# Kernel tuning notes

Hardware: AMD Instinct MI355X
Metric: run time of the kernel (lower is better)

## Reference

```python
import jax, jax.numpy as jnp
import numpy as np

N = 50000      # nodes
E = 800000     # edges
D = 128        # in_dim == out_dim
H = 8          # heads
DH = D // H    # head dim = 16
BN_EPS = 1e-5


def batch_norm(x, gamma, beta):
    # BatchNorm1d in training mode: biased variance over the node/batch axis.
    mu = jnp.mean(x, axis=0)
    var = jnp.mean((x - mu) ** 2, axis=0)
    return (x - mu) * jax.lax.rsqrt(var + BN_EPS) * gamma + beta


def setup_inputs() -> dict:
    key = jax.random.key(0)
    ks = jax.random.split(key, 16)
    inp = {
        'src': jax.random.randint(ks[0], (E,), 0, N),
        'dst': jax.random.randint(ks[1], (E,), 0, N),
        'h': jax.random.normal(ks[2], (N, D), jnp.float32),
        'e': jax.random.normal(ks[3], (E, D), jnp.float32),
        'h_in': jax.random.normal(ks[4], (N, D), jnp.float32),  # unused: overwritten by h in forward
        # attention projections (bias=False)
        'Wq': jax.random.normal(ks[5], (D, D), jnp.float32) / np.sqrt(D),
        'Wk': jax.random.normal(ks[6], (D, D), jnp.float32) / np.sqrt(D),
        'Wv': jax.random.normal(ks[7], (D, D), jnp.float32) / np.sqrt(D),
        'We': jax.random.normal(ks[8], (D, D), jnp.float32) / np.sqrt(D),
        # sdp_layer (bias=True)
        'W_sdp': jax.random.normal(ks[9], (D, D), jnp.float32) / np.sqrt(D),
        'b_sdp': jnp.zeros((D,), jnp.float32),
        # FFN out_h / out_h_2
        'W_h1': jax.random.normal(ks[10], (D, 2 * D), jnp.float32) / np.sqrt(D),
        'b_h1': jnp.zeros((2 * D,), jnp.float32),
        'W_h2': jax.random.normal(ks[11], (2 * D, D), jnp.float32) / np.sqrt(2 * D),
        'b_h2': jnp.zeros((D,), jnp.float32),
        # batch_norm_1 (shared across both BN applications)
        'bn_gamma': jnp.ones((D,), jnp.float32),
        'bn_beta': jnp.zeros((D,), jnp.float32),
    }
    return inp


def reference(src, dst, h, e, h_in, Wq, Wk, Wv, We, W_sdp, b_sdp,
              W_h1, b_h1, W_h2, b_h2, bn_gamma, bn_beta):
    h_res = h  # h_in = h inside forward

    # --- MultiHeadAttention (default path: all edges real, sum aggregation) ---
    q = (h @ Wq).reshape(N, H, DH)
    k = (h @ Wk).reshape(N, H, DH)
    v = (h @ Wv).reshape(N, H, DH)   # v = v_linear(h_in) with h_in == h
    ef = (e @ We).reshape(E, H, DH)

    # src_dot_dst -> scaling -> imp_exp_attn: elementwise K_src*Q_dst / sqrt(dh) * E
    score = (k[src] * q[dst]) / np.sqrt(DH) * ef          # [E, H, DH]
    # exp('score'): exp(clamp(sum_d score, -5, 5)), keepdim
    score_soft = jnp.exp(jnp.clip(score.sum(-1), -5.0, 5.0))[..., None]  # [E, H, 1]

    aV = jax.ops.segment_sum(v[src] * score_soft, dst, num_segments=N)   # [N, H, DH]
    z = jax.ops.segment_sum(score_soft, dst, num_segments=N)             # [N, H, 1]
    h_attn = (aV / (z + 1e-6)).reshape(N, D)

    # --- EncoderLayer post-attention (dropout=0 -> identity) ---
    hx = h_attn @ W_sdp + b_sdp
    hx = h_res + hx
    hx = batch_norm(hx, bn_gamma, bn_beta)

    h_in2 = hx
    ff = jax.nn.relu(hx @ W_h1 + b_h1) @ W_h2 + b_h2
    hx = h_in2 + ff
    hx = batch_norm(hx, bn_gamma, bn_beta)

    # edge_learning=False: e returned unchanged
    return hx, e
```

## Files before the change

kernel.cpp:

```cpp
#include <hip/hip_runtime.h>
#include <hip/hip_bf16.h>
#include <math.h>

#define N_NODES 50000
#define E_EDGES 800000
#define D_DIM   128
#define H_HEADS 8

typedef __attribute__((ext_vector_type(8))) short short8;
typedef __attribute__((ext_vector_type(4))) float f32x4;
typedef unsigned int   uint_t;
typedef unsigned short ushort_t;

static __device__ __forceinline__ float4 ldg4(const float* p) {
    return *reinterpret_cast<const float4*>(p);
}
static __device__ __forceinline__ ushort_t f2bf(float x) {
    union { float f; uint_t u; } v; v.f = x;
    uint_t r = v.u + 0x7fffu + ((v.u >> 16) & 1u);
    return (ushort_t)(r >> 16);
}
static __device__ __forceinline__ uint_t pk(float lo, float hi) {
    return (uint_t)f2bf(lo) | ((uint_t)f2bf(hi) << 16);
}

__global__ void hist_kernel(const int* __restrict__ dst, int* __restrict__ hist) {
    int i = blockIdx.x * blockDim.x + threadIdx.x;
    if (i < E_EDGES) atomicAdd(&hist[dst[i]], 1);
}

__global__ __launch_bounds__(1024) void scan_kernel(const int* __restrict__ cnt,
                                                    int* __restrict__ start,
                                                    int* __restrict__ cursor) {
    __shared__ int sh[1024];
    const int t = threadIdx.x;
    const int CPT = (N_NODES + 1023) / 1024;
    int lo = t * CPT;
    int hi = lo + CPT; if (hi > N_NODES) hi = N_NODES; if (lo > N_NODES) lo = N_NODES;
    int s = 0;
    for (int i = lo; i < hi; i++) s += cnt[i];
    sh[t] = s;
    __syncthreads();
    for (int off = 1; off < 1024; off <<= 1) {
        int v = (t >= off) ? sh[t - off] : 0;
        __syncthreads();
        sh[t] += v;
        __syncthreads();
    }
    int run = sh[t] - s;
    for (int i = lo; i < hi; i++) {
        start[i]  = run;
        cursor[i] = run;
        run += cnt[i];
    }
    if (t == 1023) start[N_NODES] = sh[1023];
}

__global__ void scatter_kernel(const int* __restrict__ dst, int* __restrict__ cursor,
                               int* __restrict__ eids) {
    int i = blockIdx.x * blockDim.x + threadIdx.x;
    if (i < E_EDGES) {
        int p = atomicAdd(&cursor[dst[i]], 1);
        eids[p] = i;
    }
}

__global__ __launch_bounds__(256) void prep_weights(const float* __restrict__ Wq,
                                                    const float* __restrict__ Wk,
                                                    const float* __restrict__ Wv,
                                                    const float* __restrict__ We,
                                                    const float* __restrict__ Wsdp,
                                                    const float* __restrict__ Wh1,
                                                    const float* __restrict__ Wh2,
                                                    ushort_t* __restrict__ prep) {
    const int b = blockIdx.x;
    const float* W; int ld, cb, kc;
    if (b < 6)       { W = (b < 2 ? Wq : (b < 4 ? Wk : Wv)); ld = 128; cb = 0; kc = b & 1; }
    else if (b < 8)  { W = We;   ld = 128; cb = 0;            kc = b - 6; }
    else if (b < 10) { W = Wsdp; ld = 128; cb = 0;            kc = b - 8; }
    else if (b < 14) { W = Wh1;  ld = 256; cb = (b - 10) >> 1; kc = (b - 10) & 1; }
    else             { W = Wh2;  ld = 128; cb = 0;            kc = b - 14; }
    char* tile = (char*)(prep + (size_t)b * 8192);
    for (int i = threadIdx.x; i < 8192; i += 256) {
        int col = i >> 6, kl = i & 63;
        int k = kc * 64 + kl;
        float v = W[(size_t)k * ld + cb * 128 + col];
        int byte = (col * 128 + kl * 2) ^ ((col & 7) << 4);
        *(ushort_t*)(tile + byte) = f2bf(v);
    }
}

__global__ __launch_bounds__(256) void gemm_bf16(const float* __restrict__ A,
                                                 int M, int K,
                                                 const ushort_t* __restrict__ Bt, int nkc,
                                                 const float* __restrict__ bias,
                                                 const float* __restrict__ resid,
                                                 float* __restrict__ C, int ldc,
                                                 size_t cbStride, int doRelu) {
    __shared__ __align__(16) unsigned char As[16384];
    __shared__ __align__(16) unsigned char Bs[16384];
    const int tid  = threadIdx.x;
    const int lane = tid & 63;
    const int wid  = tid >> 6;
    const int wr   = wid >> 1;
    const int wc   = wid & 1;
    const int cb   = blockIdx.y;
    const int row0 = blockIdx.x * 128;

    f32x4 acc[4][4];
#pragma unroll
    for (int i = 0; i < 4; i++)
#pragma unroll
        for (int j = 0; j < 4; j++) acc[i][j] = (f32x4){0.f, 0.f, 0.f, 0.f};

    for (int kc = 0; kc < nkc; kc++) {
        __syncthreads();
        {
            int row = tid >> 1;
            int kl0 = (tid & 1) * 32;
            int gr  = row0 + row;
            float4 v4[8];
            if (gr < M) {
                const float* ap = &A[(size_t)gr * K + kc * 64 + kl0];
#pragma unroll
                for (int j = 0; j < 8; j++) v4[j] = ldg4(ap + 4 * j);
            } else {
#pragma unroll
                for (int j = 0; j < 8; j++) v4[j] = make_float4(0.f, 0.f, 0.f, 0.f);
            }
            int s = (row & 7) << 4;
#pragma unroll
            for (int j = 0; j < 4; j++) {
                uint4 w;
                w.x = pk(v4[2 * j].x, v4[2 * j].y);
                w.y = pk(v4[2 * j].z, v4[2 * j].w);
                w.z = pk(v4[2 * j + 1].x, v4[2 * j + 1].y);
                w.w = pk(v4[2 * j + 1].z, v4[2 * j + 1].w);
                int byte = (row * 128 + (kl0 + 8 * j) * 2) ^ s;
                *(uint4*)(As + byte) = w;
            }
        }
        {
            const uint4* gB = (const uint4*)(Bt + (size_t)(cb * nkc + kc) * 8192);
#pragma unroll
            for (int j = 0; j < 4; j++) {
                int idx = j * 256 + tid;
                ((uint4*)Bs)[idx] = gB[idx];
            }
        }
        __syncthreads();
#pragma unroll
        for (int k0 = 0; k0 < 64; k0 += 32) {
            short8 a[4], b[4];
#pragma unroll
            for (int mi = 0; mi < 4; mi++) {
                int row = wr * 64 + mi * 16 + (lane & 15);
                int byte = (row * 128 + k0 * 2 + (lane >> 4) * 16) ^ ((row & 7) << 4);
                a[mi] = *(const short8*)(As + byte);
            }
#pragma unroll
            for (int ni = 0; ni < 4; ni++) {
                int col = wc * 64 + ni * 16 + (lane & 15);
                int byte = (col * 128 + k0 * 2 + (lane >> 4) * 16) ^ ((col & 7) << 4);
                b[ni] = *(const short8*)(Bs + byte);
            }
#pragma unroll
            for (int mi = 0; mi < 4; mi++)
#pragma unroll
                for (int ni = 0; ni < 4; ni++)
                    acc[mi][ni] = __builtin_amdgcn_mfma_f32_16x16x32_bf16(a[mi], b[ni], acc[mi][ni], 0, 0, 0);
        }
    }
#pragma unroll
    for (int mi = 0; mi < 4; mi++) {
#pragma unroll
        for (int r = 0; r < 4; r++) {
            int row = row0 + wr * 64 + mi * 16 + ((lane >> 4) << 2) + r;
            if (row < M) {
#pragma unroll
                for (int ni = 0; ni < 4; ni++) {
                    int col = wc * 64 + ni * 16 + (lane & 15);
                    float v = acc[mi][ni][r];
                    if (bias) v += bias[cb * 128 + col];
                    if (doRelu) v = fmaxf(v, 0.f);
                    if (resid) v += resid[(size_t)row * ldc + col];
                    C[cb * cbStride + (size_t)row * ldc + col] = v;
                }
            }
        }
    }
}

__global__ __launch_bounds__(512) void edge_mfma(const float* __restrict__ e,
                                                 const int* __restrict__ src,
                                                 const int* __restrict__ dst,
                                                 const float* __restrict__ Qm,
                                                 const float* __restrict__ Km,
                                                 const ushort_t* __restrict__ WeT,
                                                 float* __restrict__ S,
                                                 float* __restrict__ out_e) {
    __shared__ __align__(16) unsigned char Asm[16384];
    __shared__ __align__(16) unsigned char Bsm[32768];
    const int tid  = threadIdx.x;
    const int lane = tid & 63;
    const int wid  = tid >> 6;
    const int wr   = wid >> 2;
    const int wc   = wid & 3;
    const int e0   = blockIdx.x * 64;

    {
        int row = tid >> 3;
        int c0  = (tid & 7) * 16;
        const float* ep = &e[(size_t)(e0 + row) * 128 + c0];
        float*       op = &out_e[(size_t)(e0 + row) * 128 + c0];
        float4 v4[4];
#pragma unroll
        for (int j = 0; j < 4; j++) v4[j] = ldg4(ep + 4 * j);
#pragma unroll
        for (int j = 0; j < 4; j++) *(float4*)(op + 4 * j) = v4[j];
        int chunk = c0 >> 6;
        int klb   = (c0 & 63) * 2;
        int s     = (row & 7) << 4;
        uint4 w0, w1;
        w0.x = pk(v4[0].x, v4[0].y); w0.y = pk(v4[0].z, v4[0].w);
        w0.z = pk(v4[1].x, v4[1].y); w0.w = pk(v4[1].z, v4[1].w);
        w1.x = pk(v4[2].x, v4[2].y); w1.y = pk(v4[2].z, v4[2].w);
        w1.z = pk(v4[3].x, v4[3].y); w1.w = pk(v4[3].z, v4[3].w);
        *(uint4*)(Asm + chunk * 8192 + ((row * 128 + klb) ^ s))      = w0;
        *(uint4*)(Asm + chunk * 8192 + ((row * 128 + klb + 16) ^ s)) = w1;
    }
    {
        const uint4* gB = (const uint4*)WeT;
#pragma unroll
        for (int j = 0; j < 4; j++) {
            int idx = j * 512 + tid;
            ((uint4*)Bsm)[idx] = gB[idx];
        }
    }
    __syncthreads();

    f32x4 acc[2][2];
#pragma unroll
    for (int i = 0; i < 2; i++)
#pragma unroll
        for (int j = 0; j < 2; j++) acc[i][j] = (f32x4){0.f, 0.f, 0.f, 0.f};

#pragma unroll
    for (int k0 = 0; k0 < 128; k0 += 32) {
        int chunk = k0 >> 6;
        int klb   = (k0 & 63) * 2;
        short8 a[2], b[2];
#pragma unroll
        for (int mi = 0; mi < 2; mi++) {
            int row = wr * 32 + mi * 16 + (lane & 15);
            int byte = chunk * 8192 + ((row * 128 + klb + (lane >> 4) * 16) ^ ((row & 7) << 4));
            a[mi] = *(const short8*)(Asm + byte);
        }
#pragma unroll
        for (int ni = 0; ni < 2; ni++) {
            int col = wc * 32 + ni * 16 + (lane & 15);
            int byte = chunk * 16384 + ((col * 128 + klb + (lane >> 4) * 16) ^ ((col & 7) << 4));
            b[ni] = *(const short8*)(Bsm + byte);
        }
#pragma unroll
        for (int mi = 0; mi < 2; mi++)
#pragma unroll
            for (int ni = 0; ni < 2; ni++)
                acc[mi][ni] = __builtin_amdgcn_mfma_f32_16x16x32_bf16(a[mi], b[ni], acc[mi][ni], 0, 0, 0);
    }

#pragma unroll
    for (int mi = 0; mi < 2; mi++) {
        int rows[4], sidx[4], didx[4];
#pragma unroll
        for (int r = 0; r < 4; r++) {
            rows[r] = e0 + wr * 32 + mi * 16 + ((lane >> 4) << 2) + r;
            sidx[r] = src[rows[r]];
            didx[r] = dst[rows[r]];
        }
#pragma unroll
        for (int ni = 0; ni < 2; ni++) {
            int head = wc * 2 + ni;
            int col  = head * 16 + (lane & 15);
            float pv[4];
#pragma unroll
            for (int r = 0; r < 4; r++) {
                float kv = Km[(size_t)sidx[r] * 128 + col];
                float qv = Qm[(size_t)didx[r] * 128 + col];
                pv[r] = acc[mi][ni][r] * kv * qv;
            }
#pragma unroll
            for (int off = 1; off < 16; off <<= 1)
#pragma unroll
                for (int r = 0; r < 4; r++) pv[r] += __shfl_xor(pv[r], off, 64);
            if ((lane & 15) == 0) {
#pragma unroll
                for (int r = 0; r < 4; r++) {
                    float v = 0.25f * pv[r];
                    v = fminf(fmaxf(v, -5.f), 5.f);
                    S[(size_t)head * E_EDGES + rows[r]] = __expf(v);
                }
            }
        }
    }
}

__global__ __launch_bounds__(128) void agg_kernel(const float* __restrict__ V,
                                                  const float* __restrict__ S,
                                                  const int* __restrict__ start,
                                                  const int* __restrict__ eids,
                                                  const int* __restrict__ src,
                                                  float* __restrict__ HA) {
    const int n = blockIdx.x;
    const int t = threadIdx.x;
    const int h = t >> 4;
    const int s0 = start[n];
    const int s1 = start[n + 1];
    float acc = 0.f, z = 0.f;
    for (int i = s0; i < s1; i++) {
        int eid = eids[i];
        float sv = S[(size_t)h * E_EDGES + eid];
        float vv = V[(size_t)src[eid] * 128 + t];
        acc = fmaf(sv, vv, acc);
        z += sv;
    }
    HA[(size_t)n * 128 + t] = acc / (z + 1e-6f);
}

__global__ __launch_bounds__(256) void bn_stats(const float* __restrict__ X,
                                                float* __restrict__ sums) {
    __shared__ float s1[256], s2[256];
    const int tid = threadIdx.x;
    float a1 = 0.f, a2 = 0.f;
    const size_t total = (size_t)N_NODES * 128;
    for (size_t i = (size_t)blockIdx.x * 256 + tid; i < total; i += (size_t)gridDim.x * 256) {
        float v = X[i];
        a1 += v;
        a2 += v * v;
    }
    s1[tid] = a1; s2[tid] = a2;
    __syncthreads();
    if (tid < 128) {
        a1 = s1[tid] + s1[tid + 128];
        a2 = s2[tid] + s2[tid + 128];
        atomicAdd(&sums[tid], a1);
        atomicAdd(&sums[128 + tid], a2);
    }
}

__global__ void bn_finalize(const float* __restrict__ sums, float* __restrict__ mu_rstd) {
    int c = threadIdx.x;
    float mu  = sums[c] * (1.f / (float)N_NODES);
    float var = sums[128 + c] * (1.f / (float)N_NODES) - mu * mu;
    mu_rstd[c]       = mu;
    mu_rstd[128 + c] = rsqrtf(var + 1e-5f);
}

__global__ __launch_bounds__(256) void bn_apply(const float* __restrict__ X,
                                                const float* __restrict__ mu_rstd,
                                                const float* __restrict__ gamma,
                                                const float* __restrict__ beta,
                                                float* __restrict__ Y) {
    const size_t total = (size_t)N_NODES * 128;
    const size_t step = (size_t)gridDim.x * blockDim.x * 4;
    for (size_t i = ((size_t)blockIdx.x * blockDim.x + threadIdx.x) * 4; i < total; i += step) {
        float4 x = ldg4(&X[i]);
        int c = (int)(i & 127);
        float4 y;
        y.x = (x.x - mu_rstd[c + 0]) * mu_rstd[128 + c + 0] * gamma[c + 0] + beta[c + 0];
        y.y = (x.y - mu_rstd[c + 1]) * mu_rstd[128 + c + 1] * gamma[c + 1] + beta[c + 1];
        y.z = (x.z - mu_rstd[c + 2]) * mu_rstd[128 + c + 2] * gamma[c + 2] + beta[c + 2];
        y.w = (x.w - mu_rstd[c + 3]) * mu_rstd[128 + c + 3] * gamma[c + 3] + beta[c + 3];
        *reinterpret_cast<float4*>(&Y[i]) = y;
    }
}

extern "C" void kernel_launch(void* const* d_in, const int* in_sizes, int n_in,
                              void* d_out, int out_size, void* d_ws, size_t ws_size,
                              hipStream_t stream) {
    (void)in_sizes; (void)n_in; (void)out_size; (void)ws_size;
    const int*   src   = (const int*)d_in[0];
    const int*   dst   = (const int*)d_in[1];
    const float* h     = (const float*)d_in[2];
    const float* e     = (const float*)d_in[3];
    const float* Wq    = (const float*)d_in[5];
    const float* Wk    = (const float*)d_in[6];
    const float* Wv    = (const float*)d_in[7];
    const float* We    = (const float*)d_in[8];
    const float* Wsdp  = (const float*)d_in[9];
    const float* bsdp  = (const float*)d_in[10];
    const float* Wh1   = (const float*)d_in[11];
    const float* bh1   = (const float*)d_in[12];
    const float* Wh2   = (const float*)d_in[13];
    const float* bh2   = (const float*)d_in[14];
    const float* gamma = (const float*)d_in[15];
    const float* beta  = (const float*)d_in[16];
    float* out = (float*)d_out;

    float* ws = (float*)d_ws;
    const size_t NM = (size_t)N_NODES * 128;
    float* Qb    = ws;
    float* Kb    = ws + NM;
    float* Vb    = ws + 2 * NM;
    float* Sb    = ws + 3 * NM;
    float* T1    = ws + 4 * NM;
    float* STATS = ws + 6 * NM;
    int* hist   = (int*)(STATS + 1024);
    int* startp = hist + N_NODES;
    int* cursor = startp + N_NODES + 1;
    int* eids   = cursor + N_NODES;
    ushort_t* prep = (ushort_t*)(eids + E_EDGES);

    float* sums1 = STATS;
    float* mr1   = STATS + 256;
    float* sums2 = STATS + 512;
    float* mr2   = STATS + 768;

    prep_weights<<<18, 256, 0, stream>>>(Wq, Wk, Wv, We, Wsdp, Wh1, Wh2, prep);

    hipMemsetAsync(STATS, 0, (1024 + N_NODES) * sizeof(float), stream);

    hist_kernel<<<(E_EDGES + 255) / 256, 256, 0, stream>>>(dst, hist);
    scan_kernel<<<1, 1024, 0, stream>>>(hist, startp, cursor);
    scatter_kernel<<<(E_EDGES + 255) / 256, 256, 0, stream>>>(dst, cursor, eids);

    const int rowTiles = (N_NODES + 127) / 128;

    gemm_bf16<<<dim3(rowTiles, 3), 256, 0, stream>>>(h, N_NODES, 128, prep, 2,
                                                     nullptr, nullptr, Qb, 128, NM, 0);

    edge_mfma<<<E_EDGES / 64, 512, 0, stream>>>(e, src, dst, Qb, Kb, prep + (size_t)6 * 8192,
                                                Sb, out + NM);

    agg_kernel<<<N_NODES, 128, 0, stream>>>(Vb, Sb, startp, eids, src, Qb);

    gemm_bf16<<<dim3(rowTiles, 1), 256, 0, stream>>>(Qb, N_NODES, 128, prep + (size_t)8 * 8192, 2,
                                                     bsdp, h, Kb, 128, 0, 0);

    bn_stats<<<512, 256, 0, stream>>>(Kb, sums1);
    bn_finalize<<<1, 128, 0, stream>>>(sums1, mr1);
    bn_apply<<<2048, 256, 0, stream>>>(Kb, mr1, gamma, beta, Vb);

    gemm_bf16<<<dim3(rowTiles, 2), 256, 0, stream>>>(Vb, N_NODES, 128, prep + (size_t)10 * 8192, 2,
                                                     bh1, nullptr, T1, 256, 128, 1);
    gemm_bf16<<<dim3(rowTiles, 1), 256, 0, stream>>>(T1, N_NODES, 256, prep + (size_t)14 * 8192, 4,
                                                     bh2, Vb, Kb, 128, 0, 0);

    bn_stats<<<512, 256, 0, stream>>>(Kb, sums2);
    bn_finalize<<<1, 128, 0, stream>>>(sums2, mr2);
    bn_apply<<<2048, 256, 0, stream>>>(Kb, mr2, gamma, beta, out);
}
```

Before: 939.6 us.

## Store edge scores in dst-sorted order and prefetch K/Q gathers before MFMA

The scatter step now records each edge's rank in the dst-sorted order plus a sorted copy of src. The edge kernel writes attention scores straight to those sorted positions, so the aggregation reads scores and source ids contiguously instead of through an eid indirection, and its loop is unrolled by four. The edge kernel is also reorganised so each wave covers 16 rows by 64 columns, with the K/Q gathers issued before the GEMM to overlap their latency. This trades a scattered write in the edge kernel for contiguous reads in aggregation, and it adds register pressure and an occupancy hint.

```diff
diff --git a/kernel.cpp b/kernel.cpp
--- a/kernel.cpp
+++ b/kernel.cpp
@@ -56,12 +56,14 @@
     if (t == 1023) start[N_NODES] = sh[1023];
 }
 
-__global__ void scatter_kernel(const int* __restrict__ dst, int* __restrict__ cursor,
-                               int* __restrict__ eids) {
+__global__ void scatter_kernel(const int* __restrict__ src, const int* __restrict__ dst,
+                               int* __restrict__ cursor,
+                               int* __restrict__ rank, int* __restrict__ srcs) {
     int i = blockIdx.x * blockDim.x + threadIdx.x;
     if (i < E_EDGES) {
         int p = atomicAdd(&cursor[dst[i]], 1);
-        eids[p] = i;
+        rank[i] = p;
+        srcs[p] = src[i];
     }
 }
 
@@ -191,31 +193,54 @@
     }
 }
 
-__global__ __launch_bounds__(512) void edge_mfma(const float* __restrict__ e,
-                                                 const int* __restrict__ src,
-                                                 const int* __restrict__ dst,
-                                                 const float* __restrict__ Qm,
-                                                 const float* __restrict__ Km,
-                                                 const ushort_t* __restrict__ WeT,
-                                                 float* __restrict__ S,
-                                                 float* __restrict__ out_e) {
+__global__ __launch_bounds__(512, 6) void edge_mfma(const float* __restrict__ e,
+                                                    const int* __restrict__ src,
+                                                    const int* __restrict__ dst,
+                                                    const float* __restrict__ Qm,
+                                                    const float* __restrict__ Km,
+                                                    const ushort_t* __restrict__ WeT,
+                                                    const int* __restrict__ rank,
+                                                    float* __restrict__ S,
+                                                    float* __restrict__ out_e) {
     __shared__ __align__(16) unsigned char Asm[16384];
     __shared__ __align__(16) unsigned char Bsm[32768];
     const int tid  = threadIdx.x;
     const int lane = tid & 63;
     const int wid  = tid >> 6;
-    const int wr   = wid >> 2;
-    const int wc   = wid & 3;
+    const int wr   = wid >> 1;
+    const int wc   = wid & 1;
     const int e0   = blockIdx.x * 64;
 
+    const int rows0 = e0 + wr * 16 + ((lane >> 4) << 2);
+    int sidx[4], didx[4], rk[4];
+#pragma unroll
+    for (int r = 0; r < 4; r++) {
+        sidx[r] = src[rows0 + r];
+        didx[r] = dst[rows0 + r];
+        rk[r]   = rank[rows0 + r];
+    }
+
+    const int row = tid >> 3;
+    const int c0  = (tid & 7) * 16;
+    const float* ep = &e[(size_t)(e0 + row) * 128 + c0];
+    float4 v4[4];
+#pragma unroll
+    for (int j = 0; j < 4; j++) v4[j] = ldg4(ep + 4 * j);
+
+    float kq[4][4];
+#pragma unroll
+    for (int ni = 0; ni < 4; ni++) {
+        const int col = (wc * 4 + ni) * 16 + (lane & 15);
+#pragma unroll
+        for (int r = 0; r < 4; r++) {
+            float kv = Km[(size_t)sidx[r] * 128 + col];
+            float qv = Qm[(size_t)didx[r] * 128 + col];
+            kq[ni][r] = kv * qv * 0.25f;
+        }
+    }
+
     {
-        int row = tid >> 3;
-        int c0  = (tid & 7) * 16;
-        const float* ep = &e[(size_t)(e0 + row) * 128 + c0];
-        float*       op = &out_e[(size_t)(e0 + row) * 128 + c0];
-        float4 v4[4];
-#pragma unroll
-        for (int j = 0; j < 4; j++) v4[j] = ldg4(ep + 4 * j);
+        float* op = &out_e[(size_t)(e0 + row) * 128 + c0];
 #pragma unroll
         for (int j = 0; j < 4; j++) *(float4*)(op + 4 * j) = v4[j];
         int chunk = c0 >> 6;
@@ -239,67 +264,44 @@
     }
     __syncthreads();
 
-    f32x4 acc[2][2];
-#pragma unroll
-    for (int i = 0; i < 2; i++)
-#pragma unroll
-        for (int j = 0; j < 2; j++) acc[i][j] = (f32x4){0.f, 0.f, 0.f, 0.f};
+    f32x4 acc[4];
+#pragma unroll
+    for (int i = 0; i < 4; i++) acc[i] = (f32x4){0.f, 0.f, 0.f, 0.f};
 
 #pragma unroll
     for (int k0 = 0; k0 < 128; k0 += 32) {
         int chunk = k0 >> 6;
         int klb   = (k0 & 63) * 2;
-        short8 a[2], b[2];
-#pragma unroll
-        for (int mi = 0; mi < 2; mi++) {
-            int row = wr * 32 + mi * 16 + (lane & 15);
-            int byte = chunk * 8192 + ((row * 128 + klb + (lane >> 4) * 16) ^ ((row & 7) << 4));
-            a[mi] = *(const short8*)(Asm + byte);
-        }
-#pragma unroll
-        for (int ni = 0; ni < 2; ni++) {
-            int col = wc * 32 + ni * 16 + (lane & 15);
+        short8 a;
+        {
+            int arow = wr * 16 + (lane & 15);
+            int byte = chunk * 8192 + ((arow * 128 + klb + (lane >> 4) * 16) ^ ((arow & 7) << 4));
+            a = *(const short8*)(Asm + byte);
+        }
+#pragma unroll
+        for (int ni = 0; ni < 4; ni++) {
+            int col = wc * 64 + ni * 16 + (lane & 15);
             int byte = chunk * 16384 + ((col * 128 + klb + (lane >> 4) * 16) ^ ((col & 7) << 4));
-            b[ni] = *(const short8*)(Bsm + byte);
-        }
-#pragma unroll
-        for (int mi = 0; mi < 2; mi++)
-#pragma unroll
-            for (int ni = 0; ni < 2; ni++)
-                acc[mi][ni] = __builtin_amdgcn_mfma_f32_16x16x32_bf16(a[mi], b[ni], acc[mi][ni], 0, 0, 0);
-    }
-
-#pragma unroll
-    for (int mi = 0; mi < 2; mi++) {
-        int rows[4], sidx[4], didx[4];
-#pragma unroll
-        for (int r = 0; r < 4; r++) {
-            rows[r] = e0 + wr * 32 + mi * 16 + ((lane >> 4) << 2) + r;
-            sidx[r] = src[rows[r]];
-            didx[r] = dst[rows[r]];
-        }
-#pragma unroll
-        for (int ni = 0; ni < 2; ni++) {
-            int head = wc * 2 + ni;
-            int col  = head * 16 + (lane & 15);
-            float pv[4];
+            short8 b = *(const short8*)(Bsm + byte);
+            acc[ni] = __builtin_amdgcn_mfma_f32_16x16x32_bf16(a, b, acc[ni], 0, 0, 0);
+        }
+    }
+
+#pragma unroll
+    for (int ni = 0; ni < 4; ni++) {
+        float pv[4];
+#pragma unroll
+        for (int r = 0; r < 4; r++) pv[r] = acc[ni][r] * kq[ni][r];
+#pragma unroll
+        for (int off = 1; off < 16; off <<= 1)
+#pragma unroll
+            for (int r = 0; r < 4; r++) pv[r] += __shfl_xor(pv[r], off, 64);
+        if ((lane & 15) == 0) {
+            const int head = wc * 4 + ni;
 #pragma unroll
             for (int r = 0; r < 4; r++) {
-                float kv = Km[(size_t)sidx[r] * 128 + col];
-                float qv = Qm[(size_t)didx[r] * 128 + col];
-                pv[r] = acc[mi][ni][r] * kv * qv;
-            }
-#pragma unroll
-            for (int off = 1; off < 16; off <<= 1)
-#pragma unroll
-                for (int r = 0; r < 4; r++) pv[r] += __shfl_xor(pv[r], off, 64);
-            if ((lane & 15) == 0) {
-#pragma unroll
-                for (int r = 0; r < 4; r++) {
-                    float v = 0.25f * pv[r];
-                    v = fminf(fmaxf(v, -5.f), 5.f);
-                    S[(size_t)head * E_EDGES + rows[r]] = __expf(v);
-                }
+                float v = fminf(fmaxf(pv[r], -5.f), 5.f);
+                S[(size_t)head * E_EDGES + rk[r]] = __expf(v);
             }
         }
     }
@@ -308,20 +310,31 @@
 __global__ __launch_bounds__(128) void agg_kernel(const float* __restrict__ V,
                                                   const float* __restrict__ S,
                                                   const int* __restrict__ start,
-                                                  const int* __restrict__ eids,
-                                                  const int* __restrict__ src,
+                                                  const int* __restrict__ srcs,
                                                   float* __restrict__ HA) {
     const int n = blockIdx.x;
     const int t = threadIdx.x;
     const int h = t >> 4;
     const int s0 = start[n];
     const int s1 = start[n + 1];
+    const float* Sh = S + (size_t)h * E_EDGES;
     float acc = 0.f, z = 0.f;
-    for (int i = s0; i < s1; i++) {
-        int eid = eids[i];
-        float sv = S[(size_t)h * E_EDGES + eid];
-        float vv = V[(size_t)src[eid] * 128 + t];
-        acc = fmaf(sv, vv, acc);
+    int i = s0;
+    for (; i + 4 <= s1; i += 4) {
+        int  n0 = srcs[i], n1 = srcs[i + 1], n2 = srcs[i + 2], n3 = srcs[i + 3];
+        float sv0 = Sh[i], sv1 = Sh[i + 1], sv2 = Sh[i + 2], sv3 = Sh[i + 3];
+        float v0 = V[(size_t)n0 * 128 + t];
+        float v1 = V[(size_t)n1 * 128 + t];
+        float v2 = V[(size_t)n2 * 128 + t];
+        float v3 = V[(size_t)n3 * 128 + t];
+        acc = fmaf(sv0, v0, acc); acc = fmaf(sv1, v1, acc);
+        acc = fmaf(sv2, v2, acc); acc = fmaf(sv3, v3, acc);
+        z += sv0 + sv1 + sv2 + sv3;
+    }
+    for (; i < s1; i++) {
+        int ns = srcs[i];
+        float sv = Sh[i];
+        acc = fmaf(sv, V[(size_t)ns * 128 + t], acc);
         z += sv;
     }
     HA[(size_t)n * 128 + t] = acc / (z + 1e-6f);
@@ -408,8 +421,10 @@
     int* hist   = (int*)(STATS + 1024);
     int* startp = hist + N_NODES;
     int* cursor = startp + N_NODES + 1;
-    int* eids   = cursor + N_NODES;
-    ushort_t* prep = (ushort_t*)(eids + E_EDGES);
+    ushort_t* prep = (ushort_t*)(((uintptr_t)(cursor + N_NODES) + 255) & ~(uintptr_t)255);
+
+    int* rank = (int*)T1;
+    int* srcs = rank + E_EDGES;
 
     float* sums1 = STATS;
     float* mr1   = STATS + 256;
@@ -422,7 +437,7 @@
 
     hist_kernel<<<(E_EDGES + 255) / 256, 256, 0, stream>>>(dst, hist);
     scan_kernel<<<1, 1024, 0, stream>>>(hist, startp, cursor);
-    scatter_kernel<<<(E_EDGES + 255) / 256, 256, 0, stream>>>(dst, cursor, eids);
+    scatter_kernel<<<(E_EDGES + 255) / 256, 256, 0, stream>>>(src, dst, cursor, rank, srcs);
 
     const int rowTiles = (N_NODES + 127) / 128;
 
@@ -430,9 +445,9 @@
                                                      nullptr, nullptr, Qb, 128, NM, 0);
 
     edge_mfma<<<E_EDGES / 64, 512, 0, stream>>>(e, src, dst, Qb, Kb, prep + (size_t)6 * 8192,
-                                                Sb, out + NM);
-
-    agg_kernel<<<N_NODES, 128, 0, stream>>>(Vb, Sb, startp, eids, src, Qb);
+                                                rank, Sb, out + NM);
+
+    agg_kernel<<<N_NODES, 128, 0, stream>>>(Vb, Sb, startp, srcs, Qb);
 
     gemm_bf16<<<dim3(rowTiles, 1), 256, 0, stream>>>(Qb, N_NODES, 128, prep + (size_t)8 * 8192, 2,
                                                      bsdp, h, Kb, 128, 0, 0);
```

Measured after the change: 952.5 us. Within noise of the previous version (+1.4%).

## Write edge scores in dst-sorted order and stream We fragments from global

Applied to the files above, without the earlier changes.

The scatter kernel now records each edge's sorted position (rank) and a dst-sorted copy of src. The edge kernel stages its scores in shared memory and writes them as contiguous 8-head rows at the sorted position. This lets the aggregation kernel read S and src sequentially instead of through an eids indirection, and its loop is unrolled by four for more loads in flight. The edge kernel also drops the 32KB shared B tile, reading pre-swizzled We MFMA fragments straight from global, and adds an occupancy hint; the cost is an extra rank buffer and scattered 32-byte score writes.

```diff
diff --git a/kernel.cpp b/kernel.cpp
--- a/kernel.cpp
+++ b/kernel.cpp
@@ -56,12 +56,14 @@
     if (t == 1023) start[N_NODES] = sh[1023];
 }
 
-__global__ void scatter_kernel(const int* __restrict__ dst, int* __restrict__ cursor,
-                               int* __restrict__ eids) {
+__global__ void scatter_kernel(const int* __restrict__ src, const int* __restrict__ dst,
+                               int* __restrict__ cursor,
+                               int* __restrict__ rank, int* __restrict__ srcs) {
     int i = blockIdx.x * blockDim.x + threadIdx.x;
     if (i < E_EDGES) {
         int p = atomicAdd(&cursor[dst[i]], 1);
-        eids[p] = i;
+        rank[i] = p;
+        srcs[p] = src[i];
     }
 }
 
@@ -90,6 +92,21 @@
     }
 }
 
+__global__ __launch_bounds__(256) void prep_we_frag(const float* __restrict__ We,
+                                                    ushort_t* __restrict__ WeF) {
+    int slot = blockIdx.x * 256 + threadIdx.x;
+    if (slot < 2048) {
+        int lane = slot & 63;
+        int kc   = (slot >> 6) & 3;
+        int cg   = slot >> 8;
+        int col  = cg * 16 + (lane & 15);
+        int kb   = kc * 32 + ((lane >> 4) << 3);
+#pragma unroll
+        for (int j = 0; j < 8; j++)
+            WeF[slot * 8 + j] = f2bf(We[(size_t)(kb + j) * 128 + col]);
+    }
+}
+
 __global__ __launch_bounds__(256) void gemm_bf16(const float* __restrict__ A,
                                                  int M, int K,
                                                  const ushort_t* __restrict__ Bt, int nkc,
@@ -191,16 +208,17 @@
     }
 }
 
-__global__ __launch_bounds__(512) void edge_mfma(const float* __restrict__ e,
-                                                 const int* __restrict__ src,
-                                                 const int* __restrict__ dst,
-                                                 const float* __restrict__ Qm,
-                                                 const float* __restrict__ Km,
-                                                 const ushort_t* __restrict__ WeT,
-                                                 float* __restrict__ S,
-                                                 float* __restrict__ out_e) {
+__global__ __launch_bounds__(512, 8) void edge_mfma(const float* __restrict__ e,
+                                                    const int* __restrict__ src,
+                                                    const int* __restrict__ dst,
+                                                    const float* __restrict__ Qm,
+                                                    const float* __restrict__ Km,
+                                                    const ushort_t* __restrict__ WeF,
+                                                    const int* __restrict__ rank,
+                                                    float* __restrict__ S,
+                                                    float* __restrict__ out_e) {
     __shared__ __align__(16) unsigned char Asm[16384];
-    __shared__ __align__(16) unsigned char Bsm[32768];
+    __shared__ float sm[64][8];
     const int tid  = threadIdx.x;
     const int lane = tid & 63;
     const int wid  = tid >> 6;
@@ -229,14 +247,6 @@
         *(uint4*)(Asm + chunk * 8192 + ((row * 128 + klb) ^ s))      = w0;
         *(uint4*)(Asm + chunk * 8192 + ((row * 128 + klb + 16) ^ s)) = w1;
     }
-    {
-        const uint4* gB = (const uint4*)WeT;
-#pragma unroll
-        for (int j = 0; j < 4; j++) {
-            int idx = j * 512 + tid;
-            ((uint4*)Bsm)[idx] = gB[idx];
-        }
-    }
     __syncthreads();
 
     f32x4 acc[2][2];
@@ -249,24 +259,22 @@
     for (int k0 = 0; k0 < 128; k0 += 32) {
         int chunk = k0 >> 6;
         int klb   = (k0 & 63) * 2;
-        short8 a[2], b[2];
+        int kc    = k0 >> 5;
+        short8 a[2];
 #pragma unroll
         for (int mi = 0; mi < 2; mi++) {
-            int row = wr * 32 + mi * 16 + (lane & 15);
-            int byte = chunk * 8192 + ((row * 128 + klb + (lane >> 4) * 16) ^ ((row & 7) << 4));
+            int arow = wr * 32 + mi * 16 + (lane & 15);
+            int byte = chunk * 8192 + ((arow * 128 + klb + (lane >> 4) * 16) ^ ((arow & 7) << 4));
             a[mi] = *(const short8*)(Asm + byte);
         }
 #pragma unroll
         for (int ni = 0; ni < 2; ni++) {
-            int col = wc * 32 + ni * 16 + (lane & 15);
-            int byte = chunk * 16384 + ((col * 128 + klb + (lane >> 4) * 16) ^ ((col & 7) << 4));
-            b[ni] = *(const short8*)(Bsm + byte);
-        }
-#pragma unroll
-        for (int mi = 0; mi < 2; mi++)
-#pragma unroll
-            for (int ni = 0; ni < 2; ni++)
-                acc[mi][ni] = __builtin_amdgcn_mfma_f32_16x16x32_bf16(a[mi], b[ni], acc[mi][ni], 0, 0, 0);
+            int cg = wc * 2 + ni;
+            short8 b = *(const short8*)(WeF + ((size_t)((cg * 4 + kc) * 64 + lane)) * 8);
+#pragma unroll
+            for (int mi = 0; mi < 2; mi++)
+                acc[mi][ni] = __builtin_amdgcn_mfma_f32_16x16x32_bf16(a[mi], b, acc[mi][ni], 0, 0, 0);
+        }
     }
 
 #pragma unroll
@@ -296,20 +304,26 @@
             if ((lane & 15) == 0) {
 #pragma unroll
                 for (int r = 0; r < 4; r++) {
-                    float v = 0.25f * pv[r];
-                    v = fminf(fmaxf(v, -5.f), 5.f);
-                    S[(size_t)head * E_EDGES + rows[r]] = __expf(v);
+                    float v = fminf(fmaxf(0.25f * pv[r], -5.f), 5.f);
+                    sm[rows[r] - e0][head] = __expf(v);
                 }
             }
         }
+    }
+    __syncthreads();
+    if (tid < 64) {
+        int rk = rank[e0 + tid];
+        float4 a0 = *(const float4*)&sm[tid][0];
+        float4 a1 = *(const float4*)&sm[tid][4];
+        *(float4*)&S[(size_t)rk * 8]     = a0;
+        *(float4*)&S[(size_t)rk * 8 + 4] = a1;
     }
 }
 
 __global__ __launch_bounds__(128) void agg_kernel(const float* __restrict__ V,
                                                   const float* __restrict__ S,
                                                   const int* __restrict__ start,
-                                                  const int* __restrict__ eids,
-                                                  const int* __restrict__ src,
+                                                  const int* __restrict__ srcs,
                                                   float* __restrict__ HA) {
     const int n = blockIdx.x;
     const int t = threadIdx.x;
@@ -317,11 +331,25 @@
     const int s0 = start[n];
     const int s1 = start[n + 1];
     float acc = 0.f, z = 0.f;
-    for (int i = s0; i < s1; i++) {
-        int eid = eids[i];
-        float sv = S[(size_t)h * E_EDGES + eid];
-        float vv = V[(size_t)src[eid] * 128 + t];
-        acc = fmaf(sv, vv, acc);
+    int i = s0;
+    for (; i + 4 <= s1; i += 4) {
+        int  n0 = srcs[i], n1 = srcs[i + 1], n2 = srcs[i + 2], n3 = srcs[i + 3];
+        float sv0 = S[(size_t)i * 8 + h];
+        float sv1 = S[(size_t)(i + 1) * 8 + h];
+        float sv2 = S[(size_t)(i + 2) * 8 + h];
+        float sv3 = S[(size_t)(i + 3) * 8 + h];
+        float v0 = V[(size_t)n0 * 128 + t];
+        float v1 = V[(size_t)n1 * 128 + t];
+        float v2 = V[(size_t)n2 * 128 + t];
+        float v3 = V[(size_t)n3 * 128 + t];
+        acc = fmaf(sv0, v0, acc); acc = fmaf(sv1, v1, acc);
+        acc = fmaf(sv2, v2, acc); acc = fmaf(sv3, v3, acc);
+        z += sv0 + sv1 + sv2 + sv3;
+    }
+    for (; i < s1; i++) {
+        int ns = srcs[i];
+        float sv = S[(size_t)i * 8 + h];
+        acc = fmaf(sv, V[(size_t)ns * 128 + t], acc);
         z += sv;
     }
     HA[(size_t)n * 128 + t] = acc / (z + 1e-6f);
@@ -408,8 +436,11 @@
     int* hist   = (int*)(STATS + 1024);
     int* startp = hist + N_NODES;
     int* cursor = startp + N_NODES + 1;
-    int* eids   = cursor + N_NODES;
-    ushort_t* prep = (ushort_t*)(eids + E_EDGES);
+    ushort_t* prep = (ushort_t*)(((uintptr_t)(cursor + N_NODES) + 255) & ~(uintptr_t)255);
+    ushort_t* WeF  = prep + (size_t)18 * 8192;
+
+    int* rank = (int*)T1;
+    int* srcs = rank + E_EDGES;
 
     float* sums1 = STATS;
     float* mr1   = STATS + 256;
@@ -417,22 +448,23 @@
     float* mr2   = STATS + 768;
 
     prep_weights<<<18, 256, 0, stream>>>(Wq, Wk, Wv, We, Wsdp, Wh1, Wh2, prep);
+    prep_we_frag<<<8, 256, 0, stream>>>(We, WeF);
 
     hipMemsetAsync(STATS, 0, (1024 + N_NODES) * sizeof(float), stream);
 
     hist_kernel<<<(E_EDGES + 255) / 256, 256, 0, stream>>>(dst, hist);
     scan_kernel<<<1, 1024, 0, stream>>>(hist, startp, cursor);
-    scatter_kernel<<<(E_EDGES + 255) / 256, 256, 0, stream>>>(dst, cursor, eids);
+    scatter_kernel<<<(E_EDGES + 255) / 256, 256, 0, stream>>>(src, dst, cursor, rank, srcs);
 
     const int rowTiles = (N_NODES + 127) / 128;
 
     gemm_bf16<<<dim3(rowTiles, 3), 256, 0, stream>>>(h, N_NODES, 128, prep, 2,
                                                      nullptr, nullptr, Qb, 128, NM, 0);
 
-    edge_mfma<<<E_EDGES / 64, 512, 0, stream>>>(e, src, dst, Qb, Kb, prep + (size_t)6 * 8192,
-                                                Sb, out + NM);
-
-    agg_kernel<<<N_NODES, 128, 0, stream>>>(Vb, Sb, startp, eids, src, Qb);
+    edge_mfma<<<E_EDGES / 64, 512, 0, stream>>>(e, src, dst, Qb, Kb, WeF,
+                                                rank, Sb, out + NM);
+
+    agg_kernel<<<N_NODES, 128, 0, stream>>>(Vb, Sb, startp, srcs, Qb);
 
     gemm_bf16<<<dim3(rowTiles, 1), 256, 0, stream>>>(Qb, N_NODES, 128, prep + (size_t)8 * 8192, 2,
                                                      bsdp, h, Kb, 128, 0, 0);
```

Result: faster. 858.5 us (-8.6%).
